# Optimization experiments

Hardware: AMD Instinct MI355X
Metric: run time of the kernel (lower is better)

The kernel has to match this reference:

```python
import jax, jax.numpy as jnp
import numpy as np

B, S, H, T = 64, 512, 768, 400


def setup_inputs() -> dict:
    key = jax.random.key(0)
    k1, k2 = jax.random.split(key)
    hidden = jax.random.normal(k1, (B, S, H), dtype=jnp.float32)
    # word_ids: non-decreasing piece->word map per sample, like HF tokenizer word_ids()
    word_ids = jnp.sort(jax.random.randint(k2, (B, S), 0, T), axis=-1).astype(jnp.int32)
    return {"hidden": hidden, "word_ids": word_ids, "num_tokens": T}


def reference(hidden, word_ids, num_tokens):
    # Ragged segment mean-pool: pool subword pieces into per-word reps.
    # hidden: [B, S, H] float; word_ids: [B, S] int in [0, num_tokens)
    b, s, h = hidden.shape
    # Flatten (sample, word) into one global segment id: sample*T + word
    seg = (jnp.arange(b, dtype=word_ids.dtype)[:, None] * num_tokens + word_ids).reshape(-1)
    sums = jax.ops.segment_sum(hidden.reshape(b * s, h), seg, num_segments=b * num_tokens)
    counts = jax.ops.segment_sum(jnp.ones((b * s,), hidden.dtype), seg, num_segments=b * num_tokens)
    # Words with zero pieces -> sum 0 / 1 = 0, matching torch.zeros fallback
    pooled = sums / jnp.maximum(counts, 1.0)[:, None]
    return pooled.reshape(b, num_tokens, h)
```

## Files before the change

### kernel.cpp

```cpp
#include <hip/hip_runtime.h>


#define BB 64
#define SS 512
#define HH 768
#define TT 400
#define RPB 4

__global__ __launch_bounds__(256) void bert_lattice_pool_kernel(
    const float* __restrict__ hidden,
    const int* __restrict__ word_ids,
    float* __restrict__ out)
{
    const int row0 = blockIdx.x * RPB;
    const int b    = row0 / TT;
    const int t0   = row0 - b * TT;

    __shared__ int s_w[SS];
    __shared__ int s_bounds[RPB + 1];

    const int2* wrow2 = reinterpret_cast<const int2*>(word_ids + b * SS);
    reinterpret_cast<int2*>(s_w)[threadIdx.x] = wrow2[threadIdx.x];
    __syncthreads();

    if (threadIdx.x <= RPB) {
        const int t = t0 + threadIdx.x;
        int lo = 0, hi = SS;
        while (lo < hi) {
            int mid = (lo + hi) >> 1;
            if (s_w[mid] < t) lo = mid + 1; else hi = mid;
        }
        s_bounds[threadIdx.x] = lo;
    }
    __syncthreads();

    const int wv    = threadIdx.x >> 6;
    const int lane  = threadIdx.x & 63;
    const int start = s_bounds[wv];
    const int end   = s_bounds[wv + 1];
    const int count = end - start;

    float4 acc0 = make_float4(0.f, 0.f, 0.f, 0.f);
    float4 acc1 = make_float4(0.f, 0.f, 0.f, 0.f);
    float4 acc2 = make_float4(0.f, 0.f, 0.f, 0.f);

    for (int s = start; s < end; ++s) {
        const float4* p =
            reinterpret_cast<const float4*>(hidden + ((size_t)b * SS + s) * HH);
        float4 v0 = p[lane];
        float4 v1 = p[lane + 64];
        float4 v2 = p[lane + 128];
        acc0.x += v0.x; acc0.y += v0.y; acc0.z += v0.z; acc0.w += v0.w;
        acc1.x += v1.x; acc1.y += v1.y; acc1.z += v1.z; acc1.w += v1.w;
        acc2.x += v2.x; acc2.y += v2.y; acc2.z += v2.z; acc2.w += v2.w;
    }

    const float inv = 1.0f / (float)(count > 0 ? count : 1);

    float4* o = reinterpret_cast<float4*>(out + ((size_t)(row0 + wv)) * HH);
    float4 r0 = make_float4(acc0.x * inv, acc0.y * inv, acc0.z * inv, acc0.w * inv);
    float4 r1 = make_float4(acc1.x * inv, acc1.y * inv, acc1.z * inv, acc1.w * inv);
    float4 r2 = make_float4(acc2.x * inv, acc2.y * inv, acc2.z * inv, acc2.w * inv);
    o[lane]       = r0;
    o[lane + 64]  = r1;
    o[lane + 128] = r2;
}

extern "C" void kernel_launch(void* const* d_in, const int* in_sizes, int n_in,
                              void* d_out, int out_size, void* d_ws, size_t ws_size,
                              hipStream_t stream) {
    (void)in_sizes; (void)n_in; (void)d_ws; (void)ws_size; (void)out_size;
    const float* hidden   = (const float*)d_in[0];
    const int*   word_ids = (const int*)d_in[1];
    float*       out      = (float*)d_out;

    dim3 grid((BB * TT) / RPB);
    dim3 block(256);
    bert_lattice_pool_kernel<<<grid, block, 0, stream>>>(hidden, word_ids, out);
}
```

Measured before the change: 174.9 us.

## Process five words per wave with software-prefetched row loads

Each wave now handles a run of five consecutive words instead of one, so the grid shrinks five-fold and the word_ids staging and binary search are amortized over more outputs. Inside the wave, the next hidden row is loaded before the current one is accumulated, carried across word boundaries, to overlap memory latency with the adds. The cost is fewer workgroups, less parallelism for hiding latency, and more uneven work per wave.

```diff
diff --git a/kernel.cpp b/kernel.cpp
--- a/kernel.cpp
+++ b/kernel.cpp
@@ -5,65 +5,84 @@
 #define SS 512
 #define HH 768
 #define TT 400
-#define RPB 4
+#define TB 5
+#define WAVES 4
+#define WWG (TB * WAVES)
+#define WGB (TT / WWG)
+#define NF4 (HH / 4)
 
 __global__ __launch_bounds__(256) void bert_lattice_pool_kernel(
     const float* __restrict__ hidden,
     const int* __restrict__ word_ids,
     float* __restrict__ out)
 {
-    const int row0 = blockIdx.x * RPB;
-    const int b    = row0 / TT;
-    const int t0   = row0 - b * TT;
+    const int wg  = blockIdx.x;
+    const int b   = wg / WGB;
+    const int tw0 = (wg - b * WGB) * WWG;
 
     __shared__ int s_w[SS];
-    __shared__ int s_bounds[RPB + 1];
+    __shared__ int s_bnd[WWG + 1];
+
+    const int tid = threadIdx.x;
 
     const int2* wrow2 = reinterpret_cast<const int2*>(word_ids + b * SS);
-    reinterpret_cast<int2*>(s_w)[threadIdx.x] = wrow2[threadIdx.x];
+    reinterpret_cast<int2*>(s_w)[tid] = wrow2[tid];
     __syncthreads();
 
-    if (threadIdx.x <= RPB) {
-        const int t = t0 + threadIdx.x;
+    if (tid <= WWG) {
+        const int t = tw0 + tid;
         int lo = 0, hi = SS;
         while (lo < hi) {
-            int mid = (lo + hi) >> 1;
+            const int mid = (lo + hi) >> 1;
             if (s_w[mid] < t) lo = mid + 1; else hi = mid;
         }
-        s_bounds[threadIdx.x] = lo;
+        s_bnd[tid] = lo;
     }
     __syncthreads();
 
-    const int wv    = threadIdx.x >> 6;
-    const int lane  = threadIdx.x & 63;
-    const int start = s_bounds[wv];
-    const int end   = s_bounds[wv + 1];
-    const int count = end - start;
+    const int wv   = tid >> 6;
+    const int lane = tid & 63;
+    const int i0   = wv * TB;
 
-    float4 acc0 = make_float4(0.f, 0.f, 0.f, 0.f);
-    float4 acc1 = make_float4(0.f, 0.f, 0.f, 0.f);
-    float4 acc2 = make_float4(0.f, 0.f, 0.f, 0.f);
+    int s        = s_bnd[i0];
+    const int S1 = s_bnd[i0 + TB];
 
-    for (int s = start; s < end; ++s) {
-        const float4* p =
-            reinterpret_cast<const float4*>(hidden + ((size_t)b * SS + s) * HH);
-        float4 v0 = p[lane];
-        float4 v1 = p[lane + 64];
-        float4 v2 = p[lane + 128];
-        acc0.x += v0.x; acc0.y += v0.y; acc0.z += v0.z; acc0.w += v0.w;
-        acc1.x += v1.x; acc1.y += v1.y; acc1.z += v1.z; acc1.w += v1.w;
-        acc2.x += v2.x; acc2.y += v2.y; acc2.z += v2.z; acc2.w += v2.w;
+    const float4* hbase = reinterpret_cast<const float4*>(hidden)
+                          + (size_t)(b * SS) * NF4;
+
+    float4 p0, p1, p2;
+    if (s < S1) {
+        const float4* p = hbase + (size_t)s * NF4;
+        p0 = p[lane]; p1 = p[lane + 64]; p2 = p[lane + 128];
     }
 
-    const float inv = 1.0f / (float)(count > 0 ? count : 1);
+    float4* obase = reinterpret_cast<float4*>(out)
+                    + ((size_t)b * TT + tw0 + i0) * NF4;
 
-    float4* o = reinterpret_cast<float4*>(out + ((size_t)(row0 + wv)) * HH);
-    float4 r0 = make_float4(acc0.x * inv, acc0.y * inv, acc0.z * inv, acc0.w * inv);
-    float4 r1 = make_float4(acc1.x * inv, acc1.y * inv, acc1.z * inv, acc1.w * inv);
-    float4 r2 = make_float4(acc2.x * inv, acc2.y * inv, acc2.z * inv, acc2.w * inv);
-    o[lane]       = r0;
-    o[lane + 64]  = r1;
-    o[lane + 128] = r2;
+    #pragma unroll
+    for (int i = 0; i < TB; ++i) {
+        const int e   = s_bnd[i0 + i + 1];
+        const int cnt = e - s;
+        float4 a0 = make_float4(0.f, 0.f, 0.f, 0.f);
+        float4 a1 = a0, a2 = a0;
+        while (s < e) {
+            const float4 c0 = p0, c1 = p1, c2 = p2;
+            const int sn = s + 1;
+            if (sn < S1) {
+                const float4* p = hbase + (size_t)sn * NF4;
+                p0 = p[lane]; p1 = p[lane + 64]; p2 = p[lane + 128];
+            }
+            a0.x += c0.x; a0.y += c0.y; a0.z += c0.z; a0.w += c0.w;
+            a1.x += c1.x; a1.y += c1.y; a1.z += c1.z; a1.w += c1.w;
+            a2.x += c2.x; a2.y += c2.y; a2.z += c2.z; a2.w += c2.w;
+            s = sn;
+        }
+        const float inv = 1.0f / (float)(cnt > 0 ? cnt : 1);
+        float4* o = obase + (size_t)i * NF4;
+        o[lane]       = make_float4(a0.x * inv, a0.y * inv, a0.z * inv, a0.w * inv);
+        o[lane + 64]  = make_float4(a1.x * inv, a1.y * inv, a1.z * inv, a1.w * inv);
+        o[lane + 128] = make_float4(a2.x * inv, a2.y * inv, a2.z * inv, a2.w * inv);
+    }
 }
 
 extern "C" void kernel_launch(void* const* d_in, const int* in_sizes, int n_in,
@@ -74,7 +93,7 @@
     const int*   word_ids = (const int*)d_in[1];
     float*       out      = (float*)d_out;
 
-    dim3 grid((BB * TT) / RPB);
+    dim3 grid(BB * WGB);
     dim3 block(256);
     bert_lattice_pool_kernel<<<grid, block, 0, stream>>>(hidden, word_ids, out);
 }
```

Result: slower. 180.0 us (+3.0%).

## Stream contiguous row ranges per block with double-buffered chunked loads

Applied to the files above, without the earlier changes.

Each block now handles 20 consecutive words of one sample. Three waves each own one third of the hidden dimension and walk the sample's contiguous row range, emitting a mean whenever a segment boundary is crossed. Segment bounds are computed in parallel by scanning word_ids instead of binary search. Rows are loaded in chunks of 8 into two alternating register buffers, so several loads are in flight per lane where the old loop issued dependent per-row loads. The cost is more registers, some redundant clamped loads at the tail, and divergent boundary-handling branches.

```diff
diff --git a/kernel.cpp b/kernel.cpp
--- a/kernel.cpp
+++ b/kernel.cpp
@@ -5,65 +5,108 @@
 #define SS 512
 #define HH 768
 #define TT 400
-#define RPB 4
+#define NF4 (HH / 4)
+#define W   20
+#define WGB (TT / W)
+#define NTHR 192
+#define CH  8
 
-__global__ __launch_bounds__(256) void bert_lattice_pool_kernel(
+__global__ __launch_bounds__(NTHR) void bert_lattice_pool_kernel(
     const float* __restrict__ hidden,
     const int* __restrict__ word_ids,
     float* __restrict__ out)
 {
-    const int row0 = blockIdx.x * RPB;
-    const int b    = row0 / TT;
-    const int t0   = row0 - b * TT;
+    const int blk = blockIdx.x;
+    const int b   = blk / WGB;
+    const int w0  = (blk - b * WGB) * W;
 
     __shared__ int s_w[SS];
-    __shared__ int s_bounds[RPB + 1];
+    __shared__ int s_bnd[W + 1];
+
+    const int tid = threadIdx.x;
 
     const int2* wrow2 = reinterpret_cast<const int2*>(word_ids + b * SS);
-    reinterpret_cast<int2*>(s_w)[threadIdx.x] = wrow2[threadIdx.x];
+    reinterpret_cast<int2*>(s_w)[tid] = wrow2[tid];
+    if (tid < 64) reinterpret_cast<int2*>(s_w)[NTHR + tid] = wrow2[NTHR + tid];
+    if (tid <= W) s_bnd[tid] = SS;
     __syncthreads();
 
-    if (threadIdx.x <= RPB) {
-        const int t = t0 + threadIdx.x;
-        int lo = 0, hi = SS;
-        while (lo < hi) {
-            int mid = (lo + hi) >> 1;
-            if (s_w[mid] < t) lo = mid + 1; else hi = mid;
-        }
-        s_bounds[threadIdx.x] = lo;
+    for (int s = tid; s < SS; s += NTHR) {
+        const int w  = s_w[s];
+        const int wp = (s == 0) ? -1 : s_w[s - 1];
+        int lo = wp + 1; if (lo < w0) lo = w0;
+        int hi = w;      if (hi > w0 + W) hi = w0 + W;
+        for (int t = lo; t <= hi; ++t) s_bnd[t - w0] = s;
     }
     __syncthreads();
 
-    const int wv    = threadIdx.x >> 6;
-    const int lane  = threadIdx.x & 63;
-    const int start = s_bounds[wv];
-    const int end   = s_bounds[wv + 1];
-    const int count = end - start;
+    const int wv   = tid >> 6;
+    const int lane = tid & 63;
 
-    float4 acc0 = make_float4(0.f, 0.f, 0.f, 0.f);
-    float4 acc1 = make_float4(0.f, 0.f, 0.f, 0.f);
-    float4 acc2 = make_float4(0.f, 0.f, 0.f, 0.f);
+    const int r0 = s_bnd[0];
+    const int r1 = s_bnd[W];
 
-    for (int s = start; s < end; ++s) {
-        const float4* p =
-            reinterpret_cast<const float4*>(hidden + ((size_t)b * SS + s) * HH);
-        float4 v0 = p[lane];
-        float4 v1 = p[lane + 64];
-        float4 v2 = p[lane + 128];
-        acc0.x += v0.x; acc0.y += v0.y; acc0.z += v0.z; acc0.w += v0.w;
-        acc1.x += v1.x; acc1.y += v1.y; acc1.z += v1.z; acc1.w += v1.w;
-        acc2.x += v2.x; acc2.y += v2.y; acc2.z += v2.z; acc2.w += v2.w;
+    const float4* hp = reinterpret_cast<const float4*>(hidden)
+                       + (size_t)b * SS * NF4 + wv * 64 + lane;
+    float4* op = reinterpret_cast<float4*>(out)
+                 + ((size_t)b * TT + w0) * NF4 + wv * 64 + lane;
+
+    const float4 z4 = make_float4(0.f, 0.f, 0.f, 0.f);
+
+    int t = 0;
+    while (t < W && s_bnd[t + 1] == r0) { op[(size_t)t * NF4] = z4; ++t; }
+    if (r0 >= r1) return;
+
+    int ws = r0;
+    int e  = (t < W) ? s_bnd[t + 1] : -1;
+    float4 acc = z4;
+    const int rmax = r1 - 1;
+
+#define LOADC(Bufr, base)                                             \
+    _Pragma("unroll")                                                 \
+    for (int i = 0; i < CH; ++i) {                                    \
+        int rr = (base) + i;                                          \
+        rr = rr > rmax ? rmax : rr;       \
+        Bufr[i] = hp[(size_t)rr * NF4];                               \
     }
 
-    const float inv = 1.0f / (float)(count > 0 ? count : 1);
+#define PROC(Bufr, base)                                              \
+    _Pragma("unroll")                                                 \
+    for (int i = 0; i < CH; ++i) {                                    \
+        const int rI = (base) + i;     \
+        if (rI < r1) {                                                \
+            acc.x += Bufr[i].x; acc.y += Bufr[i].y;                   \
+            acc.z += Bufr[i].z; acc.w += Bufr[i].w;                   \
+            if (rI + 1 == e) {                                        \
+                const int cnt = e - ws;                               \
+                const float inv = 1.0f / (float)cnt;                  \
+                op[(size_t)t * NF4] = make_float4(acc.x * inv,        \
+                    acc.y * inv, acc.z * inv, acc.w * inv);           \
+                acc = z4; ws = e; ++t;                                \
+                while (t < W && s_bnd[t + 1] == e) {                  \
+                    op[(size_t)t * NF4] = z4; ++t;    \
+                }                                                     \
+                e = (t < W) ? s_bnd[t + 1] : -1;                      \
+            }                                                         \
+        }                                                             \
+    }
 
-    float4* o = reinterpret_cast<float4*>(out + ((size_t)(row0 + wv)) * HH);
-    float4 r0 = make_float4(acc0.x * inv, acc0.y * inv, acc0.z * inv, acc0.w * inv);
-    float4 r1 = make_float4(acc1.x * inv, acc1.y * inv, acc1.z * inv, acc1.w * inv);
-    float4 r2 = make_float4(acc2.x * inv, acc2.y * inv, acc2.z * inv, acc2.w * inv);
-    o[lane]       = r0;
-    o[lane + 64]  = r1;
-    o[lane + 128] = r2;
+    float4 A[CH], Bf[CH];
+    int r = r0;
+    LOADC(A, r);
+    for (;;) {
+        LOADC(Bf, r + CH);
+        PROC(A, r);
+        r += CH;
+        if (r >= r1) break;
+        LOADC(A, r + CH);
+        PROC(Bf, r);
+        r += CH;
+        if (r >= r1) break;
+    }
+
+#undef LOADC
+#undef PROC
 }
 
 extern "C" void kernel_launch(void* const* d_in, const int* in_sizes, int n_in,
@@ -74,7 +117,7 @@
     const int*   word_ids = (const int*)d_in[1];
     float*       out      = (float*)d_out;
 
-    dim3 grid((BB * TT) / RPB);
-    dim3 block(256);
+    dim3 grid(BB * WGB);
+    dim3 block(NTHR);
     bert_lattice_pool_kernel<<<grid, block, 0, stream>>>(hidden, word_ids, out);
 }
```

Result: no change. 178.0 us (+1.8%).

## Precompute per-word segment bounds in a separate kernel before pooling

Applied to the files above, without the earlier changes.

Adds a small per-sample kernel that scatters each word's start offset into a workspace table, replacing the per-block reload of word_ids into shared memory and the binary searches. The pooling kernel then reads start/end directly from global memory without any syncthreads. This drops redundant shared-memory loads and barriers from 6400 blocks at the cost of an extra kernel launch and a serial dependency between the two kernels.

```diff
diff --git a/kernel.cpp b/kernel.cpp
--- a/kernel.cpp
+++ b/kernel.cpp
@@ -1,80 +1,92 @@
 #include <hip/hip_runtime.h>
 
+
+#include <stdint.h>
 
 #define BB 64
 #define SS 512
 #define HH 768
 #define TT 400
-#define RPB 4
+#define LN (TT + 1)
+#define NF4 (HH / 4)
+
+__global__ __launch_bounds__(256) void bounds_kernel(
+    const int* __restrict__ word_ids, int* __restrict__ L)
+{
+    const int b   = blockIdx.x;
+    const int tid = threadIdx.x;
+
+    __shared__ int s_w[SS];
+    __shared__ int s_L[LN];
+
+    const int2* r2 = reinterpret_cast<const int2*>(word_ids + b * SS);
+    reinterpret_cast<int2*>(s_w)[tid] = r2[tid];
+    for (int t = tid; t < LN; t += 256) s_L[t] = SS;
+    __syncthreads();
+
+    for (int s = tid; s < SS; s += 256) {
+        const int w  = s_w[s];
+        const int wp = (s == 0) ? -1 : s_w[s - 1];
+        for (int t = wp + 1; t <= w; ++t) s_L[t] = s;
+    }
+    __syncthreads();
+
+    int* Lb = L + b * LN;
+    for (int t = tid; t < LN; t += 256) Lb[t] = s_L[t];
+}
 
 __global__ __launch_bounds__(256) void bert_lattice_pool_kernel(
     const float* __restrict__ hidden,
-    const int* __restrict__ word_ids,
+    const int* __restrict__ L,
     float* __restrict__ out)
 {
-    const int row0 = blockIdx.x * RPB;
-    const int b    = row0 / TT;
-    const int t0   = row0 - b * TT;
+    const int blk  = blockIdx.x;
+    const int b    = blk / (TT / 4);
+    const int q    = blk - b * (TT / 4);
+    const int wv   = threadIdx.x >> 6;
+    const int lane = threadIdx.x & 63;
+    const int t    = q * 4 + wv;
 
-    __shared__ int s_w[SS];
-    __shared__ int s_bounds[RPB + 1];
-
-    const int2* wrow2 = reinterpret_cast<const int2*>(word_ids + b * SS);
-    reinterpret_cast<int2*>(s_w)[threadIdx.x] = wrow2[threadIdx.x];
-    __syncthreads();
-
-    if (threadIdx.x <= RPB) {
-        const int t = t0 + threadIdx.x;
-        int lo = 0, hi = SS;
-        while (lo < hi) {
-            int mid = (lo + hi) >> 1;
-            if (s_w[mid] < t) lo = mid + 1; else hi = mid;
-        }
-        s_bounds[threadIdx.x] = lo;
-    }
-    __syncthreads();
-
-    const int wv    = threadIdx.x >> 6;
-    const int lane  = threadIdx.x & 63;
-    const int start = s_bounds[wv];
-    const int end   = s_bounds[wv + 1];
+    const int* Lb   = L + b * LN + t;
+    const int start = Lb[0];
+    const int end   = Lb[1];
     const int count = end - start;
 
-    float4 acc0 = make_float4(0.f, 0.f, 0.f, 0.f);
-    float4 acc1 = make_float4(0.f, 0.f, 0.f, 0.f);
-    float4 acc2 = make_float4(0.f, 0.f, 0.f, 0.f);
+    const float4* hp = reinterpret_cast<const float4*>(hidden)
+                       + (size_t)(b * SS) * NF4;
+
+    float4 a0 = make_float4(0.f, 0.f, 0.f, 0.f);
+    float4 a1 = a0, a2 = a0;
 
     for (int s = start; s < end; ++s) {
-        const float4* p =
-            reinterpret_cast<const float4*>(hidden + ((size_t)b * SS + s) * HH);
+        const float4* p = hp + (size_t)s * NF4;
         float4 v0 = p[lane];
         float4 v1 = p[lane + 64];
         float4 v2 = p[lane + 128];
-        acc0.x += v0.x; acc0.y += v0.y; acc0.z += v0.z; acc0.w += v0.w;
-        acc1.x += v1.x; acc1.y += v1.y; acc1.z += v1.z; acc1.w += v1.w;
-        acc2.x += v2.x; acc2.y += v2.y; acc2.z += v2.z; acc2.w += v2.w;
+        a0.x += v0.x; a0.y += v0.y; a0.z += v0.z; a0.w += v0.w;
+        a1.x += v1.x; a1.y += v1.y; a1.z += v1.z; a1.w += v1.w;
+        a2.x += v2.x; a2.y += v2.y; a2.z += v2.z; a2.w += v2.w;
     }
 
     const float inv = 1.0f / (float)(count > 0 ? count : 1);
 
-    float4* o = reinterpret_cast<float4*>(out + ((size_t)(row0 + wv)) * HH);
-    float4 r0 = make_float4(acc0.x * inv, acc0.y * inv, acc0.z * inv, acc0.w * inv);
-    float4 r1 = make_float4(acc1.x * inv, acc1.y * inv, acc1.z * inv, acc1.w * inv);
-    float4 r2 = make_float4(acc2.x * inv, acc2.y * inv, acc2.z * inv, acc2.w * inv);
-    o[lane]       = r0;
-    o[lane + 64]  = r1;
-    o[lane + 128] = r2;
+    float4* o = reinterpret_cast<float4*>(out) + ((size_t)b * TT + t) * NF4;
+    o[lane]       = make_float4(a0.x * inv, a0.y * inv, a0.z * inv, a0.w * inv);
+    o[lane + 64]  = make_float4(a1.x * inv, a1.y * inv, a1.z * inv, a1.w * inv);
+    o[lane + 128] = make_float4(a2.x * inv, a2.y * inv, a2.z * inv, a2.w * inv);
 }
 
 extern "C" void kernel_launch(void* const* d_in, const int* in_sizes, int n_in,
                               void* d_out, int out_size, void* d_ws, size_t ws_size,
                               hipStream_t stream) {
-    (void)in_sizes; (void)n_in; (void)d_ws; (void)ws_size; (void)out_size;
+    (void)in_sizes; (void)n_in; (void)ws_size; (void)out_size;
     const float* hidden   = (const float*)d_in[0];
     const int*   word_ids = (const int*)d_in[1];
     float*       out      = (float*)d_out;
+    int*         L        = (int*)d_ws;
 
-    dim3 grid((BB * TT) / RPB);
-    dim3 block(256);
-    bert_lattice_pool_kernel<<<grid, block, 0, stream>>>(hidden, word_ids, out);
+    bounds_kernel<<<dim3(BB), dim3(256), 0, stream>>>(word_ids, L);
+
+    bert_lattice_pool_kernel<<<dim3(BB * TT / 4), dim3(256), 0, stream>>>(
+        hidden, L, out);
 }
```

New measurement: 176.1 us. No clear change (+0.7%).
